# Kernel optimization log

Measured on AMD Instinct MI355X. Metric: run time of the kernel, lower is better.

The kernel has to match this reference:

```python
import jax, jax.numpy as jnp
import numpy as np


def setup_inputs() -> dict:
    key = jax.random.key(0)
    k0, k1, k2, k3, k4 = jax.random.split(key, 5)
    dim, b, h, w = 256, 32, 56, 56
    x = jax.random.normal(k0, (b, dim, h, w), jnp.float32)
    # 1x1 conv qk: weight [out=dim, in=dim], bias [dim]
    qk_w = jax.random.normal(k1, (dim, dim), jnp.float32) * (1.0 / np.sqrt(dim))
    qk_b = jax.random.normal(k2, (dim,), jnp.float32) * 0.01
    # depthwise 3x3 conv pe: weight [dim, 1, 3, 3], bias [dim]
    pe_w = jax.random.normal(k3, (dim, 1, 3, 3), jnp.float32) * (1.0 / 3.0)
    pe_b = jax.random.normal(k4, (dim,), jnp.float32) * 0.01
    return {"x": x, "qk_w": qk_w, "qk_b": qk_b, "pe_w": pe_w, "pe_b": pe_b}


def reference(x, qk_w, qk_b, pe_w, pe_b):
    b, c, h, w = x.shape
    n = h * w
    d = c // 2                      # head_dim = dim // 2
    s = float(n) ** -0.5
    # 1x1 conv + (elu + 1) feature map
    qk = jnp.einsum('bchw,oc->bohw', x, qk_w) + qk_b[None, :, None, None]
    qk = jax.nn.elu(qk) + 1.0
    qk = qk.reshape(b, 2, d, n)
    q, k = qk[:, 0], qk[:, 1]       # each [b, d, n]
    v = x.reshape(b, c, n)          # [b, c, n]
    # kv outer product: (k*s) @ (v^T * s) -> [b, d, c]
    kv = jnp.einsum('bdn,bcn->bdc', k, v) * (s * s)
    # numerator q^T @ kv -> [b, n, c]
    num = jnp.einsum('bdn,bdc->bnc', q, kv)
    # denominator q^T @ mean(k, axis=-1) -> [b, n, 1]
    den = jnp.einsum('bdn,bd->bn', q, jnp.mean(k, axis=-1))[:, :, None] + 1e-6
    attn = (num / den).transpose(0, 2, 1).reshape(b, c, h, w)
    # depthwise 3x3 positional conv on v (= x)
    pe = jax.lax.conv_general_dilated(
        x, pe_w, window_strides=(1, 1), padding='SAME',
        dimension_numbers=('NCHW', 'OIHW', 'NCHW'), feature_group_count=c)
    return attn + pe + pe_b[None, :, None, None]
```

## Files before the change

### kernel.cpp

```cpp
#include <hip/hip_runtime.h>

#define B_ 32
#define C_ 256
#define D_ 128
#define HH 56
#define WW 56
#define N_ 3136
#define KSPLIT 7
#define KRANGE 448

typedef float f32x4 __attribute__((ext_vector_type(4)));
typedef short s16x8 __attribute__((ext_vector_type(8)));
typedef unsigned short u16x8 __attribute__((ext_vector_type(8)));

__device__ __forceinline__ int swz4(int r){
  return (r & 3) ^ (((r >> 2) & 1) << 1) ^ ((r >> 3) & 1);
}
__device__ __forceinline__ unsigned short f2bf(float f){
  unsigned u = __float_as_uint(f);
  u += 0x7fffu + ((u >> 16) & 1u);
  return (unsigned short)(u >> 16);
}
__device__ __forceinline__ float bf2f(unsigned short h){
  return __uint_as_float(((unsigned)h) << 16);
}
__device__ __forceinline__ float elu1(float v){
  return v > 0.f ? v + 1.f : __expf(v);
}
__device__ __forceinline__ unsigned cvtpk(float lo, float hi){
  unsigned r;
  asm("v_cvt_pk_bf16_f32 %0, %1, %2" : "=v"(r) : "v"(lo), "v"(hi));
  return r;
}

template<int R>
__device__ __forceinline__ void stage_glds(const unsigned short* gp, int ld, char* lds){
  const int tid = threadIdx.x;
  const int wid = tid >> 6;
#pragma unroll
  for (int q = 0; q < R/64; ++q){
    const int slot = q*256 + tid;
    const int r = slot >> 2, gi = slot & 3;
    const int u = gi ^ swz4(r);
    const unsigned short* ga = gp + r*ld + u*8;
    char* lb = lds + (q*256 + wid*64)*16;
    __builtin_amdgcn_global_load_lds(
        (__attribute__((address_space(1))) void*)ga,
        (__attribute__((address_space(3))) void*)lb, 16, 0, 0);
  }
}

__device__ __forceinline__ s16x8 ldsfrag(const char* lds, int r, int g){
  return *(const s16x8*)(lds + r*64 + ((g ^ swz4(r)) << 4));
}

__global__ __launch_bounds__(256) void k0_w(
    const float* __restrict__ w, unsigned short* __restrict__ wb)
{
  const int i = blockIdx.x*256 + threadIdx.x;
  float4 v = *(const float4*)(w + (size_t)i*4);
  uint2 h = {cvtpk(v.x, v.y), cvtpk(v.z, v.w)};
  *(uint2*)(wb + (size_t)i*4) = h;
}

__global__ __launch_bounds__(256) void k0_t(
    const float* __restrict__ x, unsigned short* __restrict__ xt)
{
  __shared__ float T[64][65];
  const int tid = threadIdx.x;
  const int n0 = blockIdx.x*64, c0 = blockIdx.y*64, b = blockIdx.z;
  const float* xb = x + ((size_t)b*C_ + c0)*N_ + n0;
#pragma unroll
  for (int q = 0; q < 4; ++q){
    const int cr = q*16 + (tid >> 4), nc = (tid & 15)*4;
    float4 v = *(const float4*)(xb + (size_t)cr*N_ + nc);
    T[cr][nc+0] = v.x; T[cr][nc+1] = v.y; T[cr][nc+2] = v.z; T[cr][nc+3] = v.w;
  }
  __syncthreads();
  const int nn = tid >> 2, cq = tid & 3;
  unsigned h[8];
#pragma unroll
  for (int j = 0; j < 8; ++j)
    h[j] = cvtpk(T[cq*16 + 2*j][nn], T[cq*16 + 2*j + 1][nn]);
  unsigned short* dst = xt + ((size_t)b*N_ + n0 + nn)*C_ + c0 + cq*16;
  *(uint4*)dst       = (uint4){h[0], h[1], h[2], h[3]};
  *(uint4*)(dst + 8) = (uint4){h[4], h[5], h[6], h[7]};
}

__global__ __launch_bounds__(256) void k1_qk(
    const unsigned short* __restrict__ xt, const unsigned short* __restrict__ wb,
    const float* __restrict__ bias,
    unsigned short* __restrict__ kbuf, unsigned short* __restrict__ qt)
{
  __shared__ __align__(16) char Al[256*64];
  __shared__ __align__(16) char Bl[64*64];
  const int tid = threadIdx.x, lane = tid & 63, wid = tid >> 6;
  const int n0 = blockIdx.x * 64;
  const int b  = blockIdx.y;
  const unsigned short* xtb = xt + ((size_t)b*N_ + n0)*C_;
  const int wo = wid*64;
  f32x4 acc[4][4] = {};

  for (int k0 = 0; k0 < C_; k0 += 32){
    __syncthreads();
    stage_glds<256>(wb + k0, C_, Al);
    stage_glds<64>(xtb + k0, C_, Bl);
    __syncthreads();
    s16x8 af[4], bv4[4];
#pragma unroll
    for (int m = 0; m < 4; ++m)  af[m]  = ldsfrag(Al, wo + m*16 + (lane & 15), lane >> 4);
#pragma unroll
    for (int nf = 0; nf < 4; ++nf) bv4[nf] = ldsfrag(Bl, nf*16 + (lane & 15), lane >> 4);
#pragma unroll
    for (int m = 0; m < 4; ++m)
#pragma unroll
      for (int nf = 0; nf < 4; ++nf)
        acc[m][nf] = __builtin_amdgcn_mfma_f32_16x16x32_bf16(af[m], bv4[nf], acc[m][nf], 0, 0, 0);
  }

  const int col = lane & 15, rg = lane >> 4;
  if (wid < 2){
#pragma unroll
    for (int m = 0; m < 4; ++m){
      const int db = wo + m*16 + rg*4;
      const float b0 = bias[db], b1 = bias[db+1], b2 = bias[db+2], b3 = bias[db+3];
#pragma unroll
      for (int nf = 0; nf < 4; ++nf){
        const int n = n0 + nf*16 + col;
        f32x4 a = acc[m][nf];
        uint2 hv = {cvtpk(elu1(a[0]+b0), elu1(a[1]+b1)),
                    cvtpk(elu1(a[2]+b2), elu1(a[3]+b3))};
        *(uint2*)(qt + ((size_t)b*N_ + n)*D_ + db) = hv;
      }
    }
  } else {
#pragma unroll
    for (int m = 0; m < 4; ++m)
#pragma unroll
      for (int j = 0; j < 4; ++j){
        const int d = wo - 128 + m*16 + rg*4 + j;
        const float bb = bias[128 + d];
#pragma unroll
        for (int nf = 0; nf < 4; ++nf){
          const int n = n0 + nf*16 + col;
          kbuf[((size_t)b*D_ + d)*N_ + n] = f2bf(elu1(acc[m][nf][j] + bb));
        }
      }
  }
}

__global__ __launch_bounds__(512) void k2_kv(
    const unsigned short* __restrict__ kbuf, const float* __restrict__ x,
    unsigned short* __restrict__ kvp, float* __restrict__ kmp)
{
  __shared__ __align__(16) char Al[128*64];
  __shared__ __align__(16) char Bl[256*64];
  const int tid = threadIdx.x, lane = tid & 63, wid = tid >> 6;
  const int ks = blockIdx.x;
  const int b  = blockIdx.y;
  const unsigned short* kb = kbuf + (size_t)b*D_*N_ + ks*KRANGE;
  const float* xb = x + (size_t)b*C_*N_ + ks*KRANGE;
  const int wd = (wid >> 2)*64, wc = (wid & 3)*64;
  f32x4 acc[4][4] = {};
  float kms = 0.f;
  const int sr = tid >> 2, sg = tid & 3;

  for (int t = 0; t < KRANGE/32; ++t){
    __syncthreads();
    {
      const int u = sg ^ swz4(sr);
      const unsigned short* ga = kb + (size_t)sr*N_ + t*32 + u*8;
      char* lb = Al + (wid*64)*16;
      __builtin_amdgcn_global_load_lds(
          (__attribute__((address_space(1))) void*)ga,
          (__attribute__((address_space(3))) void*)lb, 16, 0, 0);
    }
#pragma unroll
    for (int q = 0; q < 4; ++q){
      int idx = q*512 + tid;
      int cc = idx >> 3, n4 = (idx & 7)*4;
      float4 v = *(const float4*)(xb + (size_t)cc*N_ + t*32 + n4);
      uint2 h = {cvtpk(v.x, v.y), cvtpk(v.z, v.w)};
      *(uint2*)(Bl + cc*64 + ((n4*2) ^ (swz4(cc) << 4))) = h;
    }
    __syncthreads();
    s16x8 af[4], bv[4];
#pragma unroll
    for (int m = 0; m < 4; ++m)  af[m] = ldsfrag(Al, wd + m*16 + (lane & 15), lane >> 4);
#pragma unroll
    for (int cf = 0; cf < 4; ++cf) bv[cf] = ldsfrag(Bl, wc + cf*16 + (lane & 15), lane >> 4);
#pragma unroll
    for (int m = 0; m < 4; ++m)
#pragma unroll
      for (int cf = 0; cf < 4; ++cf)
        acc[m][cf] = __builtin_amdgcn_mfma_f32_16x16x32_bf16(af[m], bv[cf], acc[m][cf], 0, 0, 0);
    {
      uint2 u = *(const uint2*)(Al + sr*64 + ((sg ^ swz4(sr)) << 4));
      uint2 u2 = *(const uint2*)(Al + sr*64 + ((sg ^ swz4(sr)) << 4) + 8);
      const unsigned ua[4] = {u.x, u.y, u2.x, u2.y};
#pragma unroll
      for (int i = 0; i < 4; ++i){
        kms += bf2f((unsigned short)(ua[i] & 0xffffu));
        kms += bf2f((unsigned short)(ua[i] >> 16));
      }
    }
  }

  kms += __shfl_xor(kms, 1);
  kms += __shfl_xor(kms, 2);
  if ((tid & 3) == 0) kmp[((size_t)b*KSPLIT + ks)*D_ + sr] = kms;

  const int col = lane & 15, rg = lane >> 4;
#pragma unroll
  for (int m = 0; m < 4; ++m){
    const int d0 = wd + m*16 + rg*4;
#pragma unroll
    for (int cf = 0; cf < 4; ++cf){
      const int c = wc + cf*16 + col;
      ushort4 hv = {f2bf(acc[m][cf][0]), f2bf(acc[m][cf][1]),
                    f2bf(acc[m][cf][2]), f2bf(acc[m][cf][3])};
      *(ushort4*)(kvp + (((size_t)b*KSPLIT + ks)*C_ + c)*D_ + d0) = hv;
    }
  }
}

__global__ __launch_bounds__(256) void kr_reduce(
    const unsigned short* __restrict__ kvp, const float* __restrict__ kmp,
    unsigned short* __restrict__ kvt, float* __restrict__ km)
{
  const int tid = threadIdx.x;
  const int bx = blockIdx.x, b = blockIdx.y;
  const float sc = 1.0f/(float)N_;
#pragma unroll
  for (int it = 0; it < 2; ++it){
    const int idx = (bx*2 + it)*256 + tid;
    const int c = idx >> 4, dq = (idx & 15)*8;
    float s[8] = {};
    for (int ks = 0; ks < KSPLIT; ++ks){
      u16x8 v = *(const u16x8*)(kvp + (((size_t)b*KSPLIT + ks)*C_ + c)*D_ + dq);
#pragma unroll
      for (int i = 0; i < 8; ++i) s[i] += bf2f(v[i]);
    }
    u16x8 h;
#pragma unroll
    for (int i = 0; i < 8; ++i) h[i] = f2bf(s[i]*sc);
    *(u16x8*)(kvt + ((size_t)b*C_ + c)*D_ + dq) = h;
  }
  if (bx == 0 && tid < D_){
    float s = 0.f;
    for (int ks = 0; ks < KSPLIT; ++ks) s += kmp[((size_t)b*KSPLIT + ks)*D_ + tid];
    km[b*D_ + tid] = s*sc;
  }
}

__global__ __launch_bounds__(256) void k3_attn(
    const unsigned short* __restrict__ qt, const unsigned short* __restrict__ kvt,
    const float* __restrict__ km, unsigned short* __restrict__ attn)
{
  __shared__ __align__(16) char SM[256*64 + 64*64];
  char* Al = SM;
  char* Bl = SM + 256*64;
  unsigned short* P = (unsigned short*)SM;
  __shared__ float kms[128];
  __shared__ float dens[64];
  const int tid = threadIdx.x, lane = tid & 63, wid = tid >> 6;
  const int n0 = blockIdx.x * 64;
  const int b  = blockIdx.y;
  if (tid < 128) kms[tid] = km[b*D_ + tid];
  const unsigned short* kvb = kvt + (size_t)b*C_*D_;
  const unsigned short* qtb = qt + ((size_t)b*N_ + n0)*D_;
  const int wc = wid*64;
  f32x4 acc[4][4] = {};
  float den = 0.f;

  for (int k0 = 0; k0 < D_; k0 += 32){
    __syncthreads();
    stage_glds<256>(kvb + k0, D_, Al);
    stage_glds<64>(qtb + k0, D_, Bl);
    __syncthreads();
    s16x8 af[4], bv4[4];
#pragma unroll
    for (int m = 0; m < 4; ++m)  af[m]  = ldsfrag(Al, wc + m*16 + (lane & 15), lane >> 4);
#pragma unroll
    for (int nf = 0; nf < 4; ++nf) bv4[nf] = ldsfrag(Bl, nf*16 + (lane & 15), lane >> 4);
#pragma unroll
    for (int m = 0; m < 4; ++m)
#pragma unroll
      for (int nf = 0; nf < 4; ++nf)
        acc[m][nf] = __builtin_amdgcn_mfma_f32_16x16x32_bf16(af[m], bv4[nf], acc[m][nf], 0, 0, 0);
    {
      const int nr = tid >> 2, g = tid & 3;
      uint4 u = *(const uint4*)(Bl + nr*64 + ((g ^ swz4(nr)) << 4));
      const float* kp = kms + k0 + g*8;
      const unsigned ua[4] = {u.x, u.y, u.z, u.w};
#pragma unroll
      for (int i = 0; i < 4; ++i){
        den += bf2f((unsigned short)(ua[i] & 0xffffu)) * kp[i*2];
        den += bf2f((unsigned short)(ua[i] >> 16))     * kp[i*2 + 1];
      }
    }
  }
  den += __shfl_xor(den, 1);
  den += __shfl_xor(den, 2);
  if ((tid & 3) == 0) dens[tid >> 2] = den;
  __syncthreads();

  const int col = lane & 15, rg = lane >> 4;
  float rdv[4];
#pragma unroll
  for (int nf = 0; nf < 4; ++nf)
    rdv[nf] = 1.0f / (dens[nf*16 + col] + 1e-6f);

#pragma unroll
  for (int h = 0; h < 2; ++h){
    if ((wid >> 1) == h){
      const int lc = wc - h*128;
#pragma unroll
      for (int m = 0; m < 4; ++m)
#pragma unroll
        for (int nf = 0; nf < 4; ++nf)
#pragma unroll
          for (int j = 0; j < 4; ++j)
            P[(lc + m*16 + rg*4 + j)*72 + (nf*16 + col)] = f2bf(acc[m][nf][j] * rdv[nf]);
    }
    __syncthreads();
#pragma unroll
    for (int p = 0; p < 4; ++p){
      const int c = (tid >> 3) + p*32, ch = tid & 7;
      u16x8 v = *(const u16x8*)(P + c*72 + ch*8);
      *(u16x8*)(attn + ((size_t)b*C_ + h*128 + c)*N_ + n0 + ch*8) = v;
    }
    __syncthreads();
  }
}

__global__ __launch_bounds__(256) void k4_pe(
    const float* __restrict__ x, const unsigned short* __restrict__ attn,
    const float* __restrict__ pw, const float* __restrict__ pb,
    float* __restrict__ out)
{
  __shared__ float xs_raw[58*56 + 8];
  float* xs = xs_raw + 4;
  const int tid = threadIdx.x;
  const int ch = blockIdx.x, b = blockIdx.y;
  const float* xp = x + ((size_t)b*C_ + ch)*N_;
  if (tid < 14)      ((float4*)xs)[tid] = (float4){0.f,0.f,0.f,0.f};
  else if (tid < 28) ((float4*)xs)[784 + tid] = (float4){0.f,0.f,0.f,0.f};
  for (int i = tid; i < 784; i += 256)
    ((float4*)xs)[14 + i] = ((const float4*)xp)[i];
  const float* wp = pw + ch*9;
  float wgt[9];
#pragma unroll
  for (int i = 0; i < 9; ++i) wgt[i] = wp[i];
  const float bias = pb[ch];
  __syncthreads();
  const unsigned short* ap = attn + ((size_t)b*C_ + ch)*N_;
  float* op = out + ((size_t)b*C_ + ch)*N_;
  for (int u = tid; u < 784; u += 256) {
    const int row = u / 14, g = u - row*14;
    float o0 = bias, o1 = bias, o2 = bias, o3 = bias;
#pragma unroll
    for (int rr = 0; rr < 3; ++rr){
      const float* rp = xs + (row + rr)*56 + g*4;
      float4 cv = *(const float4*)rp;
      float lf = (g > 0)  ? rp[-1] : 0.f;
      float rt = (g < 13) ? rp[4]  : 0.f;
      const float wl = wgt[rr*3], wc_ = wgt[rr*3+1], wr = wgt[rr*3+2];
      o0 += wl*lf   + wc_*cv.x + wr*cv.y;
      o1 += wl*cv.x + wc_*cv.y + wr*cv.z;
      o2 += wl*cv.y + wc_*cv.z + wr*cv.w;
      o3 += wl*cv.z + wc_*cv.w + wr*rt;
    }
    ushort4 av = *(const ushort4*)(ap + u*4);
    float4 ov = {o0 + bf2f(av.x), o1 + bf2f(av.y), o2 + bf2f(av.z), o3 + bf2f(av.w)};
    *(float4*)(op + u*4) = ov;
  }
}

extern "C" void kernel_launch(void* const* d_in, const int* in_sizes, int n_in,
                              void* d_out, int out_size, void* d_ws, size_t ws_size,
                              hipStream_t stream) {
  (void)in_sizes; (void)n_in; (void)out_size; (void)ws_size;
  const float* x   = (const float*)d_in[0];
  const float* qkw = (const float*)d_in[1];
  const float* qkb = (const float*)d_in[2];
  const float* pew = (const float*)d_in[3];
  const float* peb = (const float*)d_in[4];
  float* out = (float*)d_out;

  unsigned short* xts  = (unsigned short*)d_ws;
  unsigned short* kbuf = xts + (size_t)B_*N_*C_;
  unsigned short* qt   = kbuf + (size_t)B_*D_*N_;
  unsigned short* kvt  = qt   + (size_t)B_*N_*D_;
  float* km  = (float*)(kvt + (size_t)B_*C_*D_);
  unsigned short* wb   = kvt;
  unsigned short* kvp  = xts;
  float* kmp = (float*)(kvp + (size_t)B_*KSPLIT*D_*C_);
  unsigned short* attn = xts;

  k0_w     <<<dim3(64),                 256, 0, stream>>>(qkw, wb);
  k0_t     <<<dim3(N_/64, C_/64, B_),   256, 0, stream>>>(x, xts);
  k1_qk    <<<dim3(N_/64, B_),          256, 0, stream>>>(xts, wb, qkb, kbuf, qt);
  k2_kv    <<<dim3(KSPLIT, B_),         512, 0, stream>>>(kbuf, x, kvp, kmp);
  kr_reduce<<<dim3(8, B_),              256, 0, stream>>>(kvp, kmp, kvt, km);
  k3_attn  <<<dim3(N_/64, B_),          256, 0, stream>>>(qt, kvt, km, attn);
  k4_pe    <<<dim3(C_, B_),             256, 0, stream>>>(x, attn, pew, peb, out);
}
```

Baseline: 170.3 us.

## Materialize a bf16 copy of x and reuse it in the kv and pe kernels

The transpose kernel now also writes a bf16 NCHW copy of x. The kv kernel then streams that copy straight into LDS with global_load_lds instead of loading fp32 and converting in registers, and the depthwise pe kernel reads the bf16 copy. The aim is to cut fp32 re-reads of x at the cost of one extra bf16 write. The new path runs only when the workspace is large enough. It also lowers the precision of the positional-conv input to bf16.

```diff
diff --git a/kernel.cpp b/kernel.cpp
--- a/kernel.cpp
+++ b/kernel.cpp
@@ -63,8 +63,10 @@
   *(uint2*)(wb + (size_t)i*4) = h;
 }
 
+template<int M>
 __global__ __launch_bounds__(256) void k0_t(
-    const float* __restrict__ x, unsigned short* __restrict__ xt)
+    const float* __restrict__ x, unsigned short* __restrict__ xt,
+    unsigned short* __restrict__ xb16)
 {
   __shared__ float T[64][65];
   const int tid = threadIdx.x;
@@ -75,6 +77,10 @@
     const int cr = q*16 + (tid >> 4), nc = (tid & 15)*4;
     float4 v = *(const float4*)(xb + (size_t)cr*N_ + nc);
     T[cr][nc+0] = v.x; T[cr][nc+1] = v.y; T[cr][nc+2] = v.z; T[cr][nc+3] = v.w;
+    if (M){
+      uint2 hh = {cvtpk(v.x, v.y), cvtpk(v.z, v.w)};
+      *(uint2*)(xb16 + ((size_t)b*C_ + c0 + cr)*N_ + n0 + nc) = hh;
+    }
   }
   __syncthreads();
   const int nn = tid >> 2, cq = tid & 3;
@@ -149,8 +155,10 @@
   }
 }
 
+template<int M>
 __global__ __launch_bounds__(512) void k2_kv(
     const unsigned short* __restrict__ kbuf, const float* __restrict__ x,
+    const unsigned short* __restrict__ xb16,
     unsigned short* __restrict__ kvp, float* __restrict__ kmp)
 {
   __shared__ __align__(16) char Al[128*64];
@@ -160,6 +168,7 @@
   const int b  = blockIdx.y;
   const unsigned short* kb = kbuf + (size_t)b*D_*N_ + ks*KRANGE;
   const float* xb = x + (size_t)b*C_*N_ + ks*KRANGE;
+  const unsigned short* xbb = xb16 + (size_t)b*C_*N_ + ks*KRANGE;
   const int wd = (wid >> 2)*64, wc = (wid & 3)*64;
   f32x4 acc[4][4] = {};
   float kms = 0.f;
@@ -175,13 +184,27 @@
           (__attribute__((address_space(1))) void*)ga,
           (__attribute__((address_space(3))) void*)lb, 16, 0, 0);
     }
-#pragma unroll
-    for (int q = 0; q < 4; ++q){
-      int idx = q*512 + tid;
-      int cc = idx >> 3, n4 = (idx & 7)*4;
-      float4 v = *(const float4*)(xb + (size_t)cc*N_ + t*32 + n4);
-      uint2 h = {cvtpk(v.x, v.y), cvtpk(v.z, v.w)};
-      *(uint2*)(Bl + cc*64 + ((n4*2) ^ (swz4(cc) << 4))) = h;
+    if (M){
+#pragma unroll
+      for (int q = 0; q < 2; ++q){
+        const int slot = q*512 + tid;
+        const int r = slot >> 2, gi = slot & 3;
+        const int u = gi ^ swz4(r);
+        const unsigned short* ga = xbb + (size_t)r*N_ + t*32 + u*8;
+        char* lb = Bl + (q*512 + wid*64)*16;
+        __builtin_amdgcn_global_load_lds(
+            (__attribute__((address_space(1))) void*)ga,
+            (__attribute__((address_space(3))) void*)lb, 16, 0, 0);
+      }
+    } else {
+#pragma unroll
+      for (int q = 0; q < 4; ++q){
+        int idx = q*512 + tid;
+        int cc = idx >> 3, n4 = (idx & 7)*4;
+        float4 v = *(const float4*)(xb + (size_t)cc*N_ + t*32 + n4);
+        uint2 h = {cvtpk(v.x, v.y), cvtpk(v.z, v.w)};
+        *(uint2*)(Bl + cc*64 + ((n4*2) ^ (swz4(cc) << 4))) = h;
+      }
     }
     __syncthreads();
     s16x8 af[4], bv[4];
@@ -334,8 +357,10 @@
   }
 }
 
+template<int M>
 __global__ __launch_bounds__(256) void k4_pe(
-    const float* __restrict__ x, const unsigned short* __restrict__ attn,
+    const float* __restrict__ x, const unsigned short* __restrict__ xb16,
+    const unsigned short* __restrict__ attn,
     const float* __restrict__ pw, const float* __restrict__ pb,
     float* __restrict__ out)
 {
@@ -343,11 +368,22 @@
   float* xs = xs_raw + 4;
   const int tid = threadIdx.x;
   const int ch = blockIdx.x, b = blockIdx.y;
-  const float* xp = x + ((size_t)b*C_ + ch)*N_;
   if (tid < 14)      ((float4*)xs)[tid] = (float4){0.f,0.f,0.f,0.f};
   else if (tid < 28) ((float4*)xs)[784 + tid] = (float4){0.f,0.f,0.f,0.f};
-  for (int i = tid; i < 784; i += 256)
-    ((float4*)xs)[14 + i] = ((const float4*)xp)[i];
+  if (M){
+    const unsigned short* xp = xb16 + ((size_t)b*C_ + ch)*N_;
+    for (int i = tid; i < 392; i += 256){
+      u16x8 v = ((const u16x8*)xp)[i];
+      float4 f0 = {bf2f(v[0]), bf2f(v[1]), bf2f(v[2]), bf2f(v[3])};
+      float4 f1 = {bf2f(v[4]), bf2f(v[5]), bf2f(v[6]), bf2f(v[7])};
+      ((float4*)xs)[14 + 2*i]     = f0;
+      ((float4*)xs)[14 + 2*i + 1] = f1;
+    }
+  } else {
+    const float* xp = x + ((size_t)b*C_ + ch)*N_;
+    for (int i = tid; i < 784; i += 256)
+      ((float4*)xs)[14 + i] = ((const float4*)xp)[i];
+  }
   const float* wp = pw + ch*9;
   float wgt[9];
 #pragma unroll
@@ -380,7 +416,7 @@
 extern "C" void kernel_launch(void* const* d_in, const int* in_sizes, int n_in,
                               void* d_out, int out_size, void* d_ws, size_t ws_size,
                               hipStream_t stream) {
-  (void)in_sizes; (void)n_in; (void)out_size; (void)ws_size;
+  (void)in_sizes; (void)n_in; (void)out_size;
   const float* x   = (const float*)d_in[0];
   const float* qkw = (const float*)d_in[1];
   const float* qkb = (const float*)d_in[2];
@@ -393,16 +429,34 @@
   unsigned short* qt   = kbuf + (size_t)B_*D_*N_;
   unsigned short* kvt  = qt   + (size_t)B_*N_*D_;
   float* km  = (float*)(kvt + (size_t)B_*C_*D_);
+  unsigned short* xb16 = (unsigned short*)(km + (size_t)B_*D_);
   unsigned short* wb   = kvt;
   unsigned short* kvp  = xts;
-  float* kmp = (float*)(kvp + (size_t)B_*KSPLIT*D_*C_);
+  float* kmp = (float*)(kvp + (size_t)B_*KSPLIT*C_*D_);
   unsigned short* attn = xts;
 
-  k0_w     <<<dim3(64),                 256, 0, stream>>>(qkw, wb);
-  k0_t     <<<dim3(N_/64, C_/64, B_),   256, 0, stream>>>(x, xts);
-  k1_qk    <<<dim3(N_/64, B_),          256, 0, stream>>>(xts, wb, qkb, kbuf, qt);
-  k2_kv    <<<dim3(KSPLIT, B_),         512, 0, stream>>>(kbuf, x, kvp, kmp);
-  kr_reduce<<<dim3(8, B_),              256, 0, stream>>>(kvp, kmp, kvt, km);
-  k3_attn  <<<dim3(N_/64, B_),          256, 0, stream>>>(qt, kvt, km, attn);
-  k4_pe    <<<dim3(C_, B_),             256, 0, stream>>>(x, attn, pew, peb, out);
-}
+  const size_t need_a = ((size_t)B_*N_*C_ + (size_t)B_*D_*N_ + (size_t)B_*N_*D_
+                       + (size_t)B_*C_*D_)*2 + (size_t)B_*D_*4
+                       + (size_t)B_*C_*N_*2;
+  const bool big = ws_size >= need_a;
+
+  k0_w<<<dim3(64), 256, 0, stream>>>(qkw, wb);
+  if (big){
+    k0_t<1><<<dim3(N_/64, C_/64, B_), 256, 0, stream>>>(x, xts, xb16);
+  } else {
+    k0_t<0><<<dim3(N_/64, C_/64, B_), 256, 0, stream>>>(x, xts, xb16);
+  }
+  k1_qk<<<dim3(N_/64, B_), 256, 0, stream>>>(xts, wb, qkb, kbuf, qt);
+  if (big){
+    k2_kv<1><<<dim3(KSPLIT, B_), 512, 0, stream>>>(kbuf, x, xb16, kvp, kmp);
+  } else {
+    k2_kv<0><<<dim3(KSPLIT, B_), 512, 0, stream>>>(kbuf, x, xb16, kvp, kmp);
+  }
+  kr_reduce<<<dim3(8, B_), 256, 0, stream>>>(kvp, kmp, kvt, km);
+  k3_attn<<<dim3(N_/64, B_), 256, 0, stream>>>(qt, kvt, km, attn);
+  if (big){
+    k4_pe<1><<<dim3(C_, B_), 256, 0, stream>>>(x, xb16, attn, pew, peb, out);
+  } else {
+    k4_pe<0><<<dim3(C_, B_), 256, 0, stream>>>(x, xb16, attn, pew, peb, out);
+  }
+}
```

Measured after the change: 165.1 us. -3.0%, faster.
